# Kernel optimization log

Hardware: AMD Instinct MI355X
Metric: run time of the kernel (lower is better)

The kernel has to match this reference:

```python
import jax, jax.numpy as jnp
import numpy as np

KS = 3
STRIDE = 1
PAD = 1


def conv2d(x, w, b=None, stride=1, pad=0):
    out = jax.lax.conv_general_dilated(
        x, w, (stride, stride), [(pad, pad), (pad, pad)],
        dimension_numbers=('NCHW', 'OIHW', 'NCHW'))
    if b is not None:
        out = out + b[None, :, None, None]
    return out


def _get_p(offset, ks, stride):
    # offset: (b, 2N, h, w); returns sampling coords p = p_0 + p_n + offset
    b, c2, h, w = offset.shape
    N = c2 // 2
    r = (ks - 1) // 2
    pn_x, pn_y = jnp.meshgrid(jnp.arange(-r, r + 1), jnp.arange(-r, r + 1), indexing='ij')
    p_n = jnp.concatenate([pn_x.reshape(-1), pn_y.reshape(-1)]).astype(offset.dtype)  # (2N,)
    p0_x, p0_y = jnp.meshgrid(jnp.arange(1, h * stride + 1, stride),
                              jnp.arange(1, w * stride + 1, stride), indexing='ij')
    p0 = jnp.concatenate([jnp.broadcast_to(p0_x, (N, h, w)),
                          jnp.broadcast_to(p0_y, (N, h, w))], 0).astype(offset.dtype)  # (2N,h,w)
    return offset + p_n[None, :, None, None] + p0[None]


def _gather_hw(src, qx, qy):
    # src: (b,c,H,W); qx,qy: (b,h,w,N) int -> (b,c,h,w,N)
    b, c, H, W = src.shape
    flat = src.reshape(b, c, H * W)
    idx = (qx * W + qy).reshape(b, -1)
    out = jax.vmap(lambda f, i: f[:, i])(flat, idx)  # (b,c,h*w*N)
    return out.reshape(b, c, qx.shape[1], qx.shape[2], qx.shape[3])


def _bilinear(src_pad, p, Hc, Wc, N):
    # p: (b,h,w,2N); clamp bounds (Hc,Wc) follow the torch code (may differ from src_pad dims)
    px, py = p[..., :N], p[..., N:]
    fx, fy = jnp.floor(px), jnp.floor(py)
    qlt_x = jnp.clip(fx, 0, Hc - 1).astype(jnp.int32)
    qlt_y = jnp.clip(fy, 0, Wc - 1).astype(jnp.int32)
    qrb_x = jnp.clip(fx + 1, 0, Hc - 1).astype(jnp.int32)
    qrb_y = jnp.clip(fy + 1, 0, Wc - 1).astype(jnp.int32)
    pxc = jnp.clip(px, 0, Hc - 1)
    pyc = jnp.clip(py, 0, Wc - 1)
    g_lt = (1 + (qlt_x - pxc)) * (1 + (qlt_y - pyc))
    g_rb = (1 - (qrb_x - pxc)) * (1 - (qrb_y - pyc))
    g_lb = (1 + (qlt_x - pxc)) * (1 - (qrb_y - pyc))
    g_rt = (1 - (qrb_x - pxc)) * (1 + (qlt_y - pyc))
    v_lt = _gather_hw(src_pad, qlt_x, qlt_y)
    v_rb = _gather_hw(src_pad, qrb_x, qrb_y)
    v_lb = _gather_hw(src_pad, qlt_x, qrb_y)
    v_rt = _gather_hw(src_pad, qrb_x, qlt_y)
    return (g_lt[:, None] * v_lt + g_rb[:, None] * v_rb
            + g_lb[:, None] * v_lb + g_rt[:, None] * v_rt)


def setup_inputs() -> dict:
    key = jax.random.key(0)
    k1, k2, k3, k4 = jax.random.split(key, 4)
    B, C, H, W = 2, 64, 128, 128
    OUTC, KSZ = 64, KS
    N = KSZ * KSZ
    x = jax.random.normal(k1, (B, C, H, W), dtype=jnp.float32)
    depth = jax.random.uniform(k2, (B, 1, H, W), dtype=jnp.float32)
    w_p = jax.random.normal(k3, (2 * N, C, 3, 3), dtype=jnp.float32) * 0.01
    b_p = jnp.zeros((2 * N,), dtype=jnp.float32)
    w_conv = jax.random.normal(k4, (OUTC, C, KSZ, KSZ), dtype=jnp.float32) * 0.05
    return {'x': x, 'depth': depth, 'w_p': w_p, 'b_p': b_p, 'w_conv': w_conv}


def reference(x, depth, w_p, b_p, w_conv):
    ks, stride, pad = KS, STRIDE, PAD
    N = ks * ks
    b, c, H, W = x.shape
    offset = conv2d(x, w_p, b_p, stride=stride, pad=1)  # (b, 2N, h, w)
    depth_pad = jnp.pad(depth, ((0, 0), (0, 0), (pad, pad), (pad, pad)))
    # pass 1: sample depth; torch clamps against UNPADDED x dims here (quirk preserved)
    p = jnp.transpose(_get_p(offset, ks, stride), (0, 2, 3, 1))  # (b,h,w,2N)
    depth_offset = _bilinear(depth_pad, p, H, W, N)  # (b,1,h,w,N)
    depth_diff = jnp.abs(depth[..., None] - depth_offset)  # (b,1,h,w,N)
    depth_weight = jnp.exp(-4.0 * depth_diff) + 0.25
    dw = jnp.concatenate([depth_weight, depth_weight], axis=-1)  # (b,1,h,w,2N)
    dw = jnp.transpose(dw, (0, 4, 2, 3, 1))[..., 0]  # (b,2N,h,w)
    offset = offset * dw
    # pass 2: sample x from padded x, clamped to padded dims
    x_pad = jnp.pad(x, ((0, 0), (0, 0), (pad, pad), (pad, pad)))
    Hp, Wp = x_pad.shape[2], x_pad.shape[3]
    p = jnp.transpose(_get_p(offset, ks, stride), (0, 2, 3, 1))
    x_offset = _bilinear(x_pad, p, Hp, Wp, N)  # (b,c,h,w,N)
    m = jnp.exp(-1.0 * depth_diff)  # (b,1,h,w,N), broadcasts over c
    x_offset = x_offset * m
    # reshape (b,c,h,w,N) -> (b,c,h*ks,w*ks) matching _reshape_x_offset
    b2, c2, h, w, _ = x_offset.shape
    xo = x_offset.reshape(b2, c2, h, w, ks, ks)
    xo = jnp.transpose(xo, (0, 1, 2, 4, 3, 5)).reshape(b2, c2, h * ks, w * ks)
    out = conv2d(xo, w_conv, None, stride=ks, pad=0)  # (b,outc,h,w)
    return out
```

## Files before the change

### kernel.cpp

```cpp
#include <hip/hip_runtime.h>
#include <math.h>


typedef __attribute__((ext_vector_type(8))) short bf16x8;
typedef __attribute__((ext_vector_type(4))) short s16x4;
typedef __attribute__((ext_vector_type(4))) float f32x4;

#define MFMA16(a, b, c) __builtin_amdgcn_mfma_f32_16x16x32_bf16((a), (b), (c), 0, 0, 0)

__device__ __forceinline__ float bf2f(short v) {
    return __uint_as_float(((unsigned)(unsigned short)v) << 16);
}
__device__ __forceinline__ short f2bf(float f) {
    unsigned u = __float_as_uint(f);
    u = u + 0x7fffu + ((u >> 16) & 1u);
    return (short)(u >> 16);
}

__global__ __launch_bounds__(256) void k_prep(const float* __restrict__ x,
                                              const float* __restrict__ w_conv,
                                              const float* __restrict__ w_p,
                                              short* __restrict__ xT,
                                              short* __restrict__ xTlo,
                                              short* __restrict__ wK,
                                              short* __restrict__ wPh,
                                              short* __restrict__ wPl) {
    __shared__ short sH[128][72];
    __shared__ short sL[128][72];
    int bid = blockIdx.x;
    int tid = threadIdx.x;
    if (bid < 256) {
        int p = tid & 127;
        int halfc = tid >> 7;
        int pix0 = bid << 7;
        int b = pix0 >> 14;
        const float* xb = x + (size_t)b * 64 * 16384 + (pix0 & 16383);
#pragma unroll
        for (int cc = 0; cc < 8; ++cc) {
            int c0 = cc * 8 + halfc * 4;
            union { short s[4]; s16x4 v; } hi, lo;
#pragma unroll
            for (int e = 0; e < 4; ++e) {
                float v = xb[(c0 + e) * 16384 + p];
                short hb = f2bf(v);
                hi.s[e] = hb;
                lo.s[e] = f2bf(v - bf2f(hb));
            }
            *reinterpret_cast<s16x4*>(&sH[p][c0]) = hi.v;
            *reinterpret_cast<s16x4*>(&sL[p][c0]) = lo.v;
        }
        __syncthreads();
        short* xTo = xT   + ((size_t)pix0 << 6);
        short* xLo = xTlo + ((size_t)pix0 << 6);
#pragma unroll
        for (int r = 0; r < 4; ++r) {
            int u = (r << 8) + tid;
            int pp = u >> 3, ch8 = u & 7;
            *reinterpret_cast<bf16x8*>(xTo + pp * 64 + ch8 * 8) =
                *reinterpret_cast<const bf16x8*>(&sH[pp][ch8 * 8]);
            *reinterpret_cast<bf16x8*>(xLo + pp * 64 + ch8 * 8) =
                *reinterpret_cast<const bf16x8*>(&sL[pp][ch8 * 8]);
        }
    } else {
        int idx = (bid - 256) * 256 + tid;
        if (idx >= 55296) return;
        if (idx < 36864) {
            int e = idx & 7, o = (idx >> 3) & 63, h = (idx >> 9) & 3, s = idx >> 11;
            int k = s * 32 + h * 8 + e;
            int n = k >> 6, c = k & 63;
            wK[idx] = f2bf(w_conv[o * 576 + c * 9 + n]);
        } else {
            int j = idx - 36864;
            int e = j & 7, m = (j >> 3) & 31, h = (j >> 8) & 3, s = j >> 10;
            int k = s * 32 + h * 8 + e;
            int t = k >> 6, c = k & 63;
            float v = (m < 18) ? w_p[m * 576 + c * 9 + t] : 0.f;
            short hb = f2bf(v);
            wPh[j] = hb;
            wPl[j] = f2bf(v - bf2f(hb));
        }
    }
}

__global__ __launch_bounds__(512, 4) void k_fused(const short* __restrict__ xT,
                                                  const short* __restrict__ xTlo,
                                                  const short* __restrict__ wPh,
                                                  const short* __restrict__ wPl,
                                                  const short* __restrict__ wK,
                                                  const float* __restrict__ depth,
                                                  const float* __restrict__ b_p,
                                                  float* __restrict__ out) {
    __shared__ __align__(16) char smem[74240];
    short* win    = (short*)smem;
    float* dwin   = (float*)(smem + 44160);
    float* part1  = (float*)(smem + 45568);
    float* pw4    = (float*)(smem + 55808);
    int*   pi4    = (int*)(smem + 65024);
    float* accred = (float*)smem;

    int tid = threadIdx.x;
    int lane = tid & 63;
    int wv = tid >> 6;
    int l15 = lane & 15, h = lane >> 4;
    int ps = wv & 3;
    int kh = wv >> 2;
    int p0 = ps << 4;
    int bid = blockIdx.x;
    int swz = (bid & 7) * 64 + (bid >> 3);
    int pb = swz << 6;
    int b = pb >> 14, i = (pb & 16383) >> 7, j0 = pb & 127;
    const short* xTb  = xT   + ((size_t)b << 20);
    const short* xTlb = xTlo + ((size_t)b << 20);
    const float* db = depth + (b << 14);

    for (int u = tid; u < 2760; u += 512) {
        int c8 = u & 7, px = u >> 3;
        int wr = px / 69, wc = px % 69;
        int r = i - 2 + wr, c = j0 - 2 + wc;
        bf16x8 v = {0, 0, 0, 0, 0, 0, 0, 0};
        if ((unsigned)r < 128u && (unsigned)c < 128u)
            v = *reinterpret_cast<const bf16x8*>(xTb + ((size_t)(r * 128 + c) << 6) + c8 * 8);
        *reinterpret_cast<bf16x8*>((char*)win + px * 128 + ((c8 ^ (px & 7)) << 4)) = v;
    }
    for (int u = tid; u < 345; u += 512) {
        int wr = u / 69, wc = u % 69;
        int r = i - 2 + wr, c = j0 - 2 + wc;
        dwin[u] = ((unsigned)r < 128u && (unsigned)c < 128u) ? db[r * 128 + c] : 0.f;
    }
    __syncthreads();

    f32x4 acc0 = {0.f, 0.f, 0.f, 0.f}, acc1 = {0.f, 0.f, 0.f, 0.f};
    int c8p = kh * 4 + h;
#pragma unroll
    for (int t = 0; t < 9; ++t) {
        int s_ = t * 2 + kh;
        int wp = (t / 3 + 1) * 69 + (p0 + l15 + t % 3 + 1);
        bf16x8 bh = *reinterpret_cast<const bf16x8*>(
            (char*)win + wp * 128 + ((c8p ^ (wp & 7)) << 4));
        int si = i + t / 3 - 1;
        int sj = j0 + p0 + l15 + t % 3 - 1;
        bf16x8 bl = {0, 0, 0, 0, 0, 0, 0, 0};
        if ((unsigned)si < 128u && (unsigned)sj < 128u)
            bl = *reinterpret_cast<const bf16x8*>(
                xTlb + ((size_t)(si * 128 + sj) << 6) + c8p * 8);
        const short* wh_ = wPh + (size_t)((s_ * 4 + h) * 32 + l15) * 8;
        const short* wl_ = wPl + (size_t)((s_ * 4 + h) * 32 + l15) * 8;
        bf16x8 ah0 = *reinterpret_cast<const bf16x8*>(wh_);
        bf16x8 ah1 = *reinterpret_cast<const bf16x8*>(wh_ + 128);
        bf16x8 al0 = *reinterpret_cast<const bf16x8*>(wl_);
        bf16x8 al1 = *reinterpret_cast<const bf16x8*>(wl_ + 128);
        acc0 = MFMA16(ah0, bh, acc0);
        acc1 = MFMA16(ah1, bh, acc1);
        acc0 = MFMA16(ah0, bl, acc0);
        acc1 = MFMA16(ah1, bl, acc1);
        acc0 = MFMA16(al0, bh, acc0);
        acc1 = MFMA16(al1, bh, acc1);
    }
    {
        float* pp = part1 + ((ps * 2 + kh) * 16 + l15) * 20;
#pragma unroll
        for (int r = 0; r < 4; ++r) {
            pp[h * 4 + r] = acc0[r];
            int o1 = 16 + h * 4 + r;
            if (o1 < 18) pp[o1] = acc1[r];
        }
    }
    __syncthreads();

    for (int u = tid; u < 576; u += 512) {
        int p = u / 9, n = u % 9;
        int pps = p >> 4, pl = p & 15;
        const float* pa = part1 + ((pps * 2) * 16 + pl) * 20;
        const float* pbm = part1 + ((pps * 2 + 1) * 16 + pl) * 20;
        float offx = pa[n] + pbm[n] + b_p[n];
        float offy = pa[9 + n] + pbm[9 + n] + b_p[9 + n];
        float gx = (float)(n / 3 - 1 + i + 1);
        float gy = (float)(n % 3 - 1 + j0 + p + 1);
        float dctr = dwin[2 * 69 + p + 2];
        float p1x = offx + gx, p1y = offy + gy;
        float fx = floorf(p1x), fy = floorf(p1y);
        float qltx = fminf(fmaxf(fx, 0.f), 127.f);
        float qlty = fminf(fmaxf(fy, 0.f), 127.f);
        float qrbx = fminf(fmaxf(fx + 1.f, 0.f), 127.f);
        float qrby = fminf(fmaxf(fy + 1.f, 0.f), 127.f);
        float pxc = fminf(fmaxf(p1x, 0.f), 127.f);
        float pyc = fminf(fmaxf(p1y, 0.f), 127.f);
        float glt = (1.f + (qltx - pxc)) * (1.f + (qlty - pyc));
        float grb = (1.f - (qrbx - pxc)) * (1.f - (qrby - pyc));
        float glb = (1.f + (qltx - pxc)) * (1.f - (qrby - pyc));
        float grt = (1.f - (qrbx - pxc)) * (1.f + (qlty - pyc));
        int ilx = (int)qltx, ily = (int)qlty, irx = (int)qrbx, iry = (int)qrby;
        auto dv = [&](int qx, int qy) -> float {
            if (qx < 1 || qx > 128 || qy < 1 || qy > 128) return 0.f;
            int r = qx - 1, c = qy - 1;
            int wr = r - (i - 2), wc = c - (j0 - 2);
            if ((unsigned)wr < 5u && (unsigned)wc < 69u) return dwin[wr * 69 + wc];
            return db[r * 128 + c];
        };
        float dof = glt * dv(ilx, ily) + grb * dv(irx, iry) + glb * dv(ilx, iry) + grt * dv(irx, ily);
        float dd = fabsf(dctr - dof);
        float dwn = expf(-4.f * dd) + 0.25f;
        float mn = expf(-dd);
        float px = offx * dwn + gx;
        float py = offy * dwn + gy;
        float fx2 = floorf(px), fy2 = floorf(py);
        float xltx = fminf(fmaxf(fx2, 0.f), 129.f);
        float xlty = fminf(fmaxf(fy2, 0.f), 129.f);
        float xrbx = fminf(fmaxf(fx2 + 1.f, 0.f), 129.f);
        float xrby = fminf(fmaxf(fy2 + 1.f, 0.f), 129.f);
        float xpxc = fminf(fmaxf(px, 0.f), 129.f);
        float xpyc = fminf(fmaxf(py, 0.f), 129.f);
        float wlt = (1.f + (xltx - xpxc)) * (1.f + (xlty - xpyc));
        float wrb = (1.f - (xrbx - xpxc)) * (1.f - (xrby - xpyc));
        float wlb = (1.f + (xltx - xpxc)) * (1.f - (xrby - xpyc));
        float wrt = (1.f - (xrbx - xpxc)) * (1.f + (xlty - xpyc));
        int jlx = (int)xltx, jly = (int)xlty, jrx = (int)xrbx, jry = (int)xrby;
        float w4o[4];
        int i4o[4];
        auto mk = [&](int qx, int qy, float gw, int slot) {
            bool ok = (qx >= 1 && qx <= 128 && qy >= 1 && qy <= 128);
            w4o[slot] = ok ? gw * mn : 0.f;
            int idx = 0;
            if (ok) {
                int r = qx - 1, c = qy - 1;
                int wr = r - (i - 2), wc = c - (j0 - 2);
                idx = ((unsigned)wr < 5u && (unsigned)wc < 69u) ? (wr * 69 + wc)
                                                                : (-1 - (r * 128 + c));
            }
            i4o[slot] = idx;
        };
        mk(jlx, jly, wlt, 0);
        mk(jrx, jry, wrb, 1);
        mk(jlx, jry, wlb, 2);
        mk(jrx, jly, wrt, 3);
        *reinterpret_cast<float4*>(pw4 + u * 4) = make_float4(w4o[0], w4o[1], w4o[2], w4o[3]);
        *reinterpret_cast<int4*>(pi4 + u * 4) = make_int4(i4o[0], i4o[1], i4o[2], i4o[3]);
    }

    const short* wkf0 = wK + (size_t)((kh * 8 + h) * 64 + l15) * 8;
    const short* wkf1 = wkf0 + 2048;
    bf16x8 f00 = *reinterpret_cast<const bf16x8*>(wkf0);
    bf16x8 f01 = *reinterpret_cast<const bf16x8*>(wkf0 + 128);
    bf16x8 f02 = *reinterpret_cast<const bf16x8*>(wkf0 + 256);
    bf16x8 f03 = *reinterpret_cast<const bf16x8*>(wkf0 + 384);
    bf16x8 f10 = *reinterpret_cast<const bf16x8*>(wkf1);
    bf16x8 f11 = *reinterpret_cast<const bf16x8*>(wkf1 + 128);
    bf16x8 f12 = *reinterpret_cast<const bf16x8*>(wkf1 + 256);
    bf16x8 f13 = *reinterpret_cast<const bf16x8*>(wkf1 + 384);
    __syncthreads();

    f32x4 A0 = {0.f, 0.f, 0.f, 0.f}, A1 = {0.f, 0.f, 0.f, 0.f};
    f32x4 A2 = {0.f, 0.f, 0.f, 0.f}, A3 = {0.f, 0.f, 0.f, 0.f};
    auto ph2_n = [&](int n, bf16x8 a00, bf16x8 a01, bf16x8 a02, bf16x8 a03,
                     bf16x8 a10, bf16x8 a11, bf16x8 a12, bf16x8 a13) {
        int uu = (p0 + l15) * 9 + n;
        float4 w4 = *reinterpret_cast<const float4*>(pw4 + uu * 4);
        int4 i4 = *reinterpret_cast<const int4*>(pi4 + uu * 4);
        const int* ip = &i4.x;
        const float* wp = &w4.x;
#pragma unroll
        for (int t = 0; t < 4; ++t) {
            int idx = ip[t];
            float w = wp[t];
            bf16x8 th0, th1;
            if (idx >= 0) {
                const char* base = (char*)win + idx * 128;
                th0 = *reinterpret_cast<const bf16x8*>(base + ((h ^ (idx & 7)) << 4));
                th1 = *reinterpret_cast<const bf16x8*>(base + (((4 + h) ^ (idx & 7)) << 4));
            } else {
                int gp = -1 - idx;
                const short* gb = xTb + ((size_t)gp << 6) + h * 8;
                th0 = *reinterpret_cast<const bf16x8*>(gb);
                th1 = *reinterpret_cast<const bf16x8*>(gb + 32);
            }
            f32x4 Z = {0.f, 0.f, 0.f, 0.f};
            f32x4 D0 = MFMA16(a00, th0, Z);
            f32x4 D1 = MFMA16(a01, th0, Z);
            f32x4 D2 = MFMA16(a02, th0, Z);
            f32x4 D3 = MFMA16(a03, th0, Z);
            D0 = MFMA16(a10, th1, D0);
            D1 = MFMA16(a11, th1, D1);
            D2 = MFMA16(a12, th1, D2);
            D3 = MFMA16(a13, th1, D3);
            A0 += w * D0;
            A1 += w * D1;
            A2 += w * D2;
            A3 += w * D3;
        }
    };
    ph2_n(kh, f00, f01, f02, f03, f10, f11, f12, f13);
    for (int n = kh + 2; n < 9; n += 2) {
        const short* wk0 = wK + (size_t)((n * 8 + h) * 64 + l15) * 8;
        const short* wk1 = wk0 + 2048;
        ph2_n(n,
              *reinterpret_cast<const bf16x8*>(wk0),
              *reinterpret_cast<const bf16x8*>(wk0 + 128),
              *reinterpret_cast<const bf16x8*>(wk0 + 256),
              *reinterpret_cast<const bf16x8*>(wk0 + 384),
              *reinterpret_cast<const bf16x8*>(wk1),
              *reinterpret_cast<const bf16x8*>(wk1 + 128),
              *reinterpret_cast<const bf16x8*>(wk1 + 256),
              *reinterpret_cast<const bf16x8*>(wk1 + 384));
    }
    __syncthreads();
    if (kh == 1) {
        float* ar = accred + (ps * 64 + lane) * 20;
        *reinterpret_cast<f32x4*>(ar)      = A0;
        *reinterpret_cast<f32x4*>(ar + 4)  = A1;
        *reinterpret_cast<f32x4*>(ar + 8)  = A2;
        *reinterpret_cast<f32x4*>(ar + 12) = A3;
    }
    __syncthreads();
    if (kh == 0) {
        const float* ar = accred + (ps * 64 + lane) * 20;
        int col = j0 + p0 + l15;
        size_t orow = ((size_t)b << 20) + ((size_t)i << 7) + col;
#pragma unroll
        for (int r = 0; r < 4; ++r) {
            out[orow + ((size_t)(h * 4 + r) << 14)]      = A0[r] + ar[r];
            out[orow + ((size_t)(16 + h * 4 + r) << 14)] = A1[r] + ar[4 + r];
            out[orow + ((size_t)(32 + h * 4 + r) << 14)] = A2[r] + ar[8 + r];
            out[orow + ((size_t)(48 + h * 4 + r) << 14)] = A3[r] + ar[12 + r];
        }
    }
}

extern "C" void kernel_launch(void* const* d_in, const int* in_sizes, int n_in,
                              void* d_out, int out_size, void* d_ws, size_t ws_size,
                              hipStream_t stream) {
    (void)in_sizes; (void)n_in; (void)out_size; (void)ws_size;
    const float* x      = (const float*)d_in[0];
    const float* depth  = (const float*)d_in[1];
    const float* w_p    = (const float*)d_in[2];
    const float* b_p    = (const float*)d_in[3];
    const float* w_conv = (const float*)d_in[4];
    float* out = (float*)d_out;

    char* wsb = (char*)d_ws;
    short* xT   = (short*)wsb;
    short* xTlo = (short*)(wsb + 4194304);
    short* wK   = (short*)(wsb + 8388608);
    short* wPh  = (short*)(wsb + 8462336);
    short* wPl  = (short*)(wsb + 8499200);

    hipLaunchKernelGGL(k_prep,  dim3(472), dim3(256), 0, stream,
                       x, w_conv, w_p, xT, xTlo, wK, wPh, wPl);
    hipLaunchKernelGGL(k_fused, dim3(512), dim3(512), 0, stream,
                       xT, xTlo, wPh, wPl, wK, depth, b_p, out);
}
```

Baseline: 35.79 us.

## Split phase-2 MFMA work by output channels instead of kernel taps across waves

```diff
diff --git a/kernel.cpp b/kernel.cpp
--- a/kernel.cpp
+++ b/kernel.cpp
@@ -96,7 +96,6 @@
     float* part1  = (float*)(smem + 45568);
     float* pw4    = (float*)(smem + 55808);
     int*   pi4    = (int*)(smem + 65024);
-    float* accred = (float*)smem;
 
     int tid = threadIdx.x;
     int lane = tid & 63;
@@ -237,22 +236,16 @@
         *reinterpret_cast<int4*>(pi4 + u * 4) = make_int4(i4o[0], i4o[1], i4o[2], i4o[3]);
     }
 
-    const short* wkf0 = wK + (size_t)((kh * 8 + h) * 64 + l15) * 8;
-    const short* wkf1 = wkf0 + 2048;
-    bf16x8 f00 = *reinterpret_cast<const bf16x8*>(wkf0);
-    bf16x8 f01 = *reinterpret_cast<const bf16x8*>(wkf0 + 128);
-    bf16x8 f02 = *reinterpret_cast<const bf16x8*>(wkf0 + 256);
-    bf16x8 f03 = *reinterpret_cast<const bf16x8*>(wkf0 + 384);
-    bf16x8 f10 = *reinterpret_cast<const bf16x8*>(wkf1);
-    bf16x8 f11 = *reinterpret_cast<const bf16x8*>(wkf1 + 128);
-    bf16x8 f12 = *reinterpret_cast<const bf16x8*>(wkf1 + 256);
-    bf16x8 f13 = *reinterpret_cast<const bf16x8*>(wkf1 + 384);
+    const short* wkp0 = wK + (size_t)((0 * 8 + h) * 64 + l15) * 8 + kh * 256;
+    const short* wkp1 = wkp0 + 2048;
+    bf16x8 f00 = *reinterpret_cast<const bf16x8*>(wkp0);
+    bf16x8 f01 = *reinterpret_cast<const bf16x8*>(wkp0 + 128);
+    bf16x8 f10 = *reinterpret_cast<const bf16x8*>(wkp1);
+    bf16x8 f11 = *reinterpret_cast<const bf16x8*>(wkp1 + 128);
     __syncthreads();
 
     f32x4 A0 = {0.f, 0.f, 0.f, 0.f}, A1 = {0.f, 0.f, 0.f, 0.f};
-    f32x4 A2 = {0.f, 0.f, 0.f, 0.f}, A3 = {0.f, 0.f, 0.f, 0.f};
-    auto ph2_n = [&](int n, bf16x8 a00, bf16x8 a01, bf16x8 a02, bf16x8 a03,
-                     bf16x8 a10, bf16x8 a11, bf16x8 a12, bf16x8 a13) {
+    auto ph2_n = [&](int n, bf16x8 a00, bf16x8 a01, bf16x8 a10, bf16x8 a11) {
         int uu = (p0 + l15) * 9 + n;
         float4 w4 = *reinterpret_cast<const float4*>(pw4 + uu * 4);
         int4 i4 = *reinterpret_cast<const int4*>(pi4 + uu * 4);
@@ -276,51 +269,31 @@
             f32x4 Z = {0.f, 0.f, 0.f, 0.f};
             f32x4 D0 = MFMA16(a00, th0, Z);
             f32x4 D1 = MFMA16(a01, th0, Z);
-            f32x4 D2 = MFMA16(a02, th0, Z);
-            f32x4 D3 = MFMA16(a03, th0, Z);
             D0 = MFMA16(a10, th1, D0);
             D1 = MFMA16(a11, th1, D1);
-            D2 = MFMA16(a12, th1, D2);
-            D3 = MFMA16(a13, th1, D3);
             A0 += w * D0;
             A1 += w * D1;
-            A2 += w * D2;
-            A3 += w * D3;
         }
     };
-    ph2_n(kh, f00, f01, f02, f03, f10, f11, f12, f13);
-    for (int n = kh + 2; n < 9; n += 2) {
-        const short* wk0 = wK + (size_t)((n * 8 + h) * 64 + l15) * 8;
+    ph2_n(0, f00, f01, f10, f11);
+    for (int n = 1; n < 9; ++n) {
+        const short* wk0 = wK + (size_t)((n * 8 + h) * 64 + l15) * 8 + kh * 256;
         const short* wk1 = wk0 + 2048;
         ph2_n(n,
               *reinterpret_cast<const bf16x8*>(wk0),
               *reinterpret_cast<const bf16x8*>(wk0 + 128),
-              *reinterpret_cast<const bf16x8*>(wk0 + 256),
-              *reinterpret_cast<const bf16x8*>(wk0 + 384),
               *reinterpret_cast<const bf16x8*>(wk1),
-              *reinterpret_cast<const bf16x8*>(wk1 + 128),
-              *reinterpret_cast<const bf16x8*>(wk1 + 256),
-              *reinterpret_cast<const bf16x8*>(wk1 + 384));
-    }
-    __syncthreads();
-    if (kh == 1) {
-        float* ar = accred + (ps * 64 + lane) * 20;
-        *reinterpret_cast<f32x4*>(ar)      = A0;
-        *reinterpret_cast<f32x4*>(ar + 4)  = A1;
-        *reinterpret_cast<f32x4*>(ar + 8)  = A2;
-        *reinterpret_cast<f32x4*>(ar + 12) = A3;
-    }
-    __syncthreads();
-    if (kh == 0) {
-        const float* ar = accred + (ps * 64 + lane) * 20;
+              *reinterpret_cast<const bf16x8*>(wk1 + 128));
+    }
+
+    {
         int col = j0 + p0 + l15;
-        size_t orow = ((size_t)b << 20) + ((size_t)i << 7) + col;
+        size_t obase = ((size_t)b << 20) + ((size_t)i << 7) + col;
+        int o0 = kh * 32 + h * 4;
 #pragma unroll
         for (int r = 0; r < 4; ++r) {
-            out[orow + ((size_t)(h * 4 + r) << 14)]      = A0[r] + ar[r];
-            out[orow + ((size_t)(16 + h * 4 + r) << 14)] = A1[r] + ar[4 + r];
-            out[orow + ((size_t)(32 + h * 4 + r) << 14)] = A2[r] + ar[8 + r];
-            out[orow + ((size_t)(48 + h * 4 + r) << 14)] = A3[r] + ar[12 + r];
+            out[obase + ((size_t)(o0 + r) << 14)]      = A0[r];
+            out[obase + ((size_t)(o0 + 16 + r) << 14)] = A1[r];
         }
     }
 }
```

Result: slower. 134.6 us (+276.1%).
